# Optimization experiments

Measured on AMD Instinct MI355X. Metric: run time of the kernel, lower is better.

Reference implementation:

```python
import jax, jax.numpy as jnp
import numpy as np

L, H, DK = 4, 8, 64
NEG = -1e9
PAD = -9999.0


def _ln(z, g, b, eps=1e-6):
    # LayerNormalization: uses unbiased std (torch default) and divides by (std + eps)
    m = jnp.mean(z, axis=-1, keepdims=True)
    s = jnp.std(z, axis=-1, keepdims=True, ddof=1)
    return g * (z - m) / (s + eps) + b


def _mha(q_in, kv_in, w, bw, pw, pb, lnp, mask):
    B, Sq, D = q_in.shape
    q = (q_in @ w[0] + bw[0]).reshape(B, Sq, H, DK).transpose(0, 2, 1, 3)
    k = (kv_in @ w[1] + bw[1]).reshape(B, -1, H, DK).transpose(0, 2, 1, 3)
    v = (kv_in @ w[2] + bw[2]).reshape(B, -1, H, DK).transpose(0, 2, 1, 3)
    scores = jnp.einsum('bhqd,bhkd->bhqk', q, k) * (1.0 / np.sqrt(DK))
    if mask is not None:
        scores = jnp.where(mask[:, None, :, :], NEG, scores)
    attn = jax.nn.softmax(scores, axis=-1)
    ctx = jnp.einsum('bhqk,bhkd->bhqd', attn, v).transpose(0, 2, 1, 3).reshape(B, Sq, H * DK)
    return _ln(q_in + ctx @ pw + pb, lnp[0], lnp[1])


def _ffn(x, w1, b1, w2, b2, lnp):
    # kernel-1 conv1d == pointwise linear; w1:[d_ff,d_model], w2:[d_model,d_ff]
    h = jax.nn.relu(jnp.einsum('bsd,fd->bsf', x, w1) + b1)
    o = jnp.einsum('bsf,df->bsd', h, w2) + b2
    return _ln(x + o, lnp[0], lnp[1])


def _forward(enc_inputs, dec_inputs, emb_w, emb_b, pos_table,
             e_qkv_w, e_qkv_b, e_pw, e_pb, e_ln1, e_w1, e_b1, e_w2, e_b2, e_ln2,
             ds_qkv_w, ds_qkv_b, ds_pw, ds_pb, d_ln1,
             dc_qkv_w, dc_qkv_b, dc_pw, dc_pb, d_ln2,
             d_w1, d_b1, d_w2, d_b2, d_ln3):
    B, Se, F = enc_inputs.shape
    Sd = dec_inputs.shape[1]
    # ConvEmbeddingLayer: kernel-1 conv producing (d_model - n_features) channels, concat with raw inputs
    enc = jnp.concatenate([enc_inputs, jnp.einsum('bsf,of->bso', enc_inputs, emb_w) + emb_b], axis=-1)
    dec = jnp.concatenate([dec_inputs, jnp.einsum('bsf,of->bso', dec_inputs, emb_w) + emb_b], axis=-1)
    # PosEncoding with full lengths -> rows 1..S of the padded table
    enc = enc + pos_table[1:Se + 1]
    dec = dec + pos_table[1:Sd + 1]
    # masks per get_attn_pad_mask / get_attn_subsequent_mask
    enc_pad = jnp.sum(enc_inputs, axis=-1) <= PAD  # [B,Se]
    dec_pad = jnp.sum(dec_inputs, axis=-1) <= PAD  # [B,Sd]
    enc_mask = jnp.broadcast_to(enc_pad[:, None, :], (B, Se, Se))
    causal = jnp.triu(jnp.ones((Sd, Sd), dtype=bool), 1)
    dec_self_mask = jnp.broadcast_to(dec_pad[:, None, :], (B, Sd, Sd)) | causal
    cross_mask = jnp.broadcast_to(enc_pad[:, None, :], (B, Sd, Se))
    for i in range(L):
        enc = _mha(enc, enc, e_qkv_w[i], e_qkv_b[i], e_pw[i], e_pb[i], e_ln1[i], enc_mask)
        enc = _ffn(enc, e_w1[i], e_b1[i], e_w2[i], e_b2[i], e_ln2[i])
    for i in range(L):
        dec = _mha(dec, dec, ds_qkv_w[i], ds_qkv_b[i], ds_pw[i], ds_pb[i], d_ln1[i], dec_self_mask)
        dec = _mha(dec, enc, dc_qkv_w[i], dc_qkv_b[i], dc_pw[i], dc_pb[i], d_ln2[i], cross_mask)
        dec = _ffn(dec, d_w1[i], d_b1[i], d_w2[i], d_b2[i], d_ln3[i])
    return dec


def setup_inputs() -> dict:
    B, Se, Sd, F, Dm, Dff = 8, 512, 512, 32, 512, 2048
    key = jax.random.key(0)
    ks = iter(jax.random.split(key, 32))
    s = 0.02

    def n(shape, sc=s):
        return jax.random.normal(next(ks), shape, jnp.float32) * sc

    # sinusoidal PosEncoding table with leading pad row
    pos = np.arange(Se, dtype=np.float64)[:, None]
    j = np.arange(Dm)[None, :]
    ang = pos / np.power(10000.0, 2.0 * (j // 2) / Dm)
    ang[:, 0::2] = np.sin(ang[:, 0::2])
    ang[:, 1::2] = np.cos(ang[:, 1::2])
    pos_table = jnp.asarray(np.concatenate([np.zeros((1, Dm)), ang]).astype(np.float32))

    ln = jnp.broadcast_to(jnp.stack([jnp.ones(Dm), jnp.zeros(Dm)]), (L, 2, Dm)).astype(jnp.float32) + 0.0
    return {
        'enc_inputs': jax.random.normal(next(ks), (B, Se, F), jnp.float32),
        'dec_inputs': jax.random.normal(next(ks), (B, Sd, F), jnp.float32),
        'emb_w': n((Dm - F, F)), 'emb_b': jnp.zeros(Dm - F, jnp.float32),
        'pos_table': pos_table,
        'e_qkv_w': n((L, 3, Dm, H * DK)), 'e_qkv_b': jnp.zeros((L, 3, H * DK), jnp.float32),
        'e_pw': n((L, H * DK, Dm)), 'e_pb': jnp.zeros((L, Dm), jnp.float32), 'e_ln1': ln,
        'e_w1': n((L, Dff, Dm)), 'e_b1': jnp.zeros((L, Dff), jnp.float32),
        'e_w2': n((L, Dm, Dff)), 'e_b2': jnp.zeros((L, Dm), jnp.float32), 'e_ln2': ln,
        'ds_qkv_w': n((L, 3, Dm, H * DK)), 'ds_qkv_b': jnp.zeros((L, 3, H * DK), jnp.float32),
        'ds_pw': n((L, H * DK, Dm)), 'ds_pb': jnp.zeros((L, Dm), jnp.float32), 'd_ln1': ln,
        'dc_qkv_w': n((L, 3, Dm, H * DK)), 'dc_qkv_b': jnp.zeros((L, 3, H * DK), jnp.float32),
        'dc_pw': n((L, H * DK, Dm)), 'dc_pb': jnp.zeros((L, Dm), jnp.float32), 'd_ln2': ln,
        'd_w1': n((L, Dff, Dm)), 'd_b1': jnp.zeros((L, Dff), jnp.float32),
        'd_w2': n((L, Dm, Dff)), 'd_b2': jnp.zeros((L, Dm), jnp.float32), 'd_ln3': ln,
    }


def reference(enc_inputs, dec_inputs, emb_w, emb_b, pos_table,
              e_qkv_w, e_qkv_b, e_pw, e_pb, e_ln1, e_w1, e_b1, e_w2, e_b2, e_ln2,
              ds_qkv_w, ds_qkv_b, ds_pw, ds_pb, d_ln1,
              dc_qkv_w, dc_qkv_b, dc_pw, dc_pb, d_ln2,
              d_w1, d_b1, d_w2, d_b2, d_ln3):
    return _forward(enc_inputs, dec_inputs, emb_w, emb_b, pos_table,
                    e_qkv_w, e_qkv_b, e_pw, e_pb, e_ln1, e_w1, e_b1, e_w2, e_b2, e_ln2,
                    ds_qkv_w, ds_qkv_b, ds_pw, ds_pb, d_ln1,
                    dc_qkv_w, dc_qkv_b, dc_pw, dc_pb, d_ln2,
                    d_w1, d_b1, d_w2, d_b2, d_ln3)
```

## Files before the change

### kernel.cpp

```cpp
#include <hip/hip_runtime.h>
#include <cstdint>
#include <cstddef>

typedef unsigned short u16;
typedef __bf16 bf16x8 __attribute__((ext_vector_type(8)));
typedef float f32x4 __attribute__((ext_vector_type(4)));

constexpr int Bz = 8, Sq = 512, Hh = 8, DKd = 64, Dm = 512, Dff = 2048, NL = 4;
constexpr int TOK = Bz * Sq;
constexpr size_t MAT = (size_t)512 * 512;
constexpr size_t EL  = (size_t)TOK * Dm;
constexpr size_t WFT = (size_t)Dff * Dm;

__device__ __forceinline__ float bf2f(u16 u) {
  union { uint32_t i; float f; } v; v.i = (uint32_t)u << 16; return v.f;
}
__device__ __forceinline__ u16 f2bf(float f) {
  union { float f; uint32_t i; } v; v.f = f;
  uint32_t i = v.i;
  i += 0x7fffu + ((i >> 16) & 1u);
  return (u16)(i >> 16);
}

__device__ __forceinline__ void gload16(const u16* g, u16* l) {
  __builtin_amdgcn_global_load_lds(
      (const __attribute__((address_space(1))) unsigned int*)g,
      (__attribute__((address_space(3))) unsigned int*)l, 16, 0, 0);
}

template<int BM, int BN, int BK>
__global__ __launch_bounds__(256)
void gemm_tile(const u16* __restrict__ A, const u16* __restrict__ Bt,
               const float* __restrict__ bias, u16* __restrict__ C,
               int K, int lda, long long sA, int ldb, long long sB,
               int ldc, long long sC, int cmode, int relu, int colofs,
               const u16* A2, int xsplit)
{
  constexpr int HM = BM / 2, HN = BN / 2, MI = HM / 16, NI = HN / 16;
  constexpr int CPR = BK / 8;
  __shared__ __align__(16) u16 As[BM * BK];
  __shared__ __align__(16) u16 Bs[BN * BK];
  const int bz = blockIdx.z;
  const u16* Abase = A;
  int colbase;
  if (A2 && (int)blockIdx.x >= xsplit) {
    Abase = A2;
    colbase = 512 + ((int)blockIdx.x - xsplit) * BN;
  } else {
    colbase = colofs + (int)blockIdx.x * BN;
  }
  const u16* Ab = Abase + (size_t)bz * (size_t)sA + (size_t)(blockIdx.y * BM) * lda;
  const u16* Bb = Bt + (size_t)bz * (size_t)sB + (size_t)colbase * ldb;
  const int tid  = threadIdx.x;
  const int lane = tid & 63;
  const int wid  = tid >> 6;
  const int l15  = lane & 15;
  const int quad = lane >> 4;
  const int wm   = wid >> 1, wn = wid & 1;

  f32x4 acc[MI][NI] = {};

  for (int k0 = 0; k0 < K; k0 += BK) {
#pragma unroll
    for (int i = 0; i < (BM * CPR) / 256; ++i) {
      const int s = tid + i * 256;
      const int row = s / CPR, cl = s % CPR;
      const int c = (cl & 8) | ((cl ^ row) & 7);
      gload16(Ab + (size_t)row * lda + k0 + c * 8, As + s * 8);
    }
#pragma unroll
    for (int i = 0; i < (BN * CPR) / 256; ++i) {
      const int s = tid + i * 256;
      const int row = s / CPR, cl = s % CPR;
      const int c = (cl & 8) | ((cl ^ row) & 7);
      gload16(Bb + (size_t)row * ldb + k0 + c * 8, Bs + s * 8);
    }
    __syncthreads();
#pragma unroll
    for (int kk = 0; kk < BK / 32; ++kk) {
      bf16x8 af[MI], bfr[NI];
#pragma unroll
      for (int mi = 0; mi < MI; ++mi) {
        const int ra = wm * HM + mi * 16 + l15;
        const int ch = kk * 4 + quad;
        const int sw = (ch & 8) | ((ch ^ ra) & 7);
        af[mi] = *(const bf16x8*)(As + ra * BK + sw * 8);
      }
#pragma unroll
      for (int ni = 0; ni < NI; ++ni) {
        const int rb = wn * HN + ni * 16 + l15;
        const int ch = kk * 4 + quad;
        const int sw = (ch & 8) | ((ch ^ rb) & 7);
        bfr[ni] = *(const bf16x8*)(Bs + rb * BK + sw * 8);
      }
#pragma unroll
      for (int mi = 0; mi < MI; ++mi)
#pragma unroll
        for (int ni = 0; ni < NI; ++ni)
          acc[mi][ni] = __builtin_amdgcn_mfma_f32_16x16x32_bf16(af[mi], bfr[ni], acc[mi][ni], 0, 0, 0);
    }
    __syncthreads();
  }

  const int rblk = blockIdx.y * BM + wm * HM + quad * 4;
#pragma unroll
  for (int ni = 0; ni < NI; ++ni) {
    const int colx = colbase + wn * HN + ni * 16 + l15;
    const float bv = bias ? bias[colx] : 0.f;
#pragma unroll
    for (int mi = 0; mi < MI; ++mi) {
#pragma unroll
      for (int r = 0; r < 4; ++r) {
        float v = acc[mi][ni][r] + bv;
        if (relu) v = fmaxf(v, 0.f);
        const int grow = rblk + mi * 16 + r;
        size_t off;
        if (cmode == 0) {
          off = (size_t)bz * (size_t)sC + (size_t)grow * ldc + colx;
        } else {
          const int sec = colx >> 9, n = colx & 511, h = n >> 6, d = n & 63;
          const int b = grow >> 9, s = grow & 511;
          if (sec == 0) v *= 0.125f;
          if (sec < 2) off = (size_t)sec * EL + (size_t)b * 262144 + (size_t)h * 32768 + (size_t)s * 64 + d;
          else         off = 2 * EL + (size_t)b * 262144 + (size_t)h * 32768 + (size_t)d * 512 + s;
        }
        C[off] = f2bf(v);
      }
    }
  }
}

__global__ __launch_bounds__(256)
void flash_attn(const u16* __restrict__ q, const u16* __restrict__ k,
                const u16* __restrict__ v, const unsigned char* __restrict__ pad,
                u16* __restrict__ ctx, int mtype)
{
  __shared__ __align__(16) u16 KVs[8192];
  __shared__ __align__(16) u16 Pw[4][2048];
  const int bh = blockIdx.y, b = bh >> 3, h = bh & 7;
  const int qt = blockIdx.x;
  const int tid = threadIdx.x, lane = tid & 63, wid = tid >> 6;
  const int l15 = lane & 15, quad = lane >> 4;
  const size_t bho = (size_t)bh * 32768;
  const int qrow = qt * 64 + wid * 16 + l15;
  const int qcd  = qt * 64 + wid * 16 + quad * 4;

  unsigned char* Ps = (unsigned char*)&Pw[0][0];
  if (tid < 128) ((uchar4*)Ps)[tid] = ((const uchar4*)(pad + b * 512))[tid];

  bf16x8 aq0 = *(const bf16x8*)(q + bho + (size_t)qrow * 64 + quad * 8);
  bf16x8 aq1 = *(const bf16x8*)(q + bho + (size_t)qrow * 64 + 32 + quad * 8);

  f32x4 S[32];
#pragma unroll
  for (int kc = 0; kc < 4; ++kc) {
    __syncthreads();
#pragma unroll
    for (int i = 0; i < 4; ++i) {
      const int s = tid + i * 256;
      const int row = s >> 3, c = (s & 7) ^ (row & 7);
      gload16(k + bho + (size_t)(kc * 128 + row) * 64 + c * 8, KVs + s * 8);
    }
    __syncthreads();
#pragma unroll
    for (int t = 0; t < 8; ++t) {
      const int sw = l15 & 7;
      bf16x8 b0 = *(const bf16x8*)(KVs + (t * 16 + l15) * 64 + (quad ^ sw) * 8);
      bf16x8 b1 = *(const bf16x8*)(KVs + (t * 16 + l15) * 64 + ((4 + quad) ^ sw) * 8);
      f32x4 z = {0.f, 0.f, 0.f, 0.f};
      z = __builtin_amdgcn_mfma_f32_16x16x32_bf16(aq0, b0, z, 0, 0, 0);
      S[kc * 8 + t] = __builtin_amdgcn_mfma_f32_16x16x32_bf16(aq1, b1, z, 0, 0, 0);
    }
  }

  unsigned pm = 0u;
#pragma unroll
  for (int t = 0; t < 32; ++t) pm |= (unsigned)(Ps[t * 16 + l15] != 0) << t;

  float inv[4];
#pragma unroll
  for (int r = 0; r < 4; ++r) {
    const int qg = qcd + r;
    float mx = -3.0e38f;
#pragma unroll
    for (int t = 0; t < 32; ++t) {
      const int col = t * 16 + l15;
      const bool m = ((pm >> t) & 1u) || (mtype == 1 && col > qg);
      const float val = m ? -1e9f : S[t][r];
      S[t][r] = val;
      mx = fmaxf(mx, val);
    }
#pragma unroll
    for (int o = 8; o > 0; o >>= 1) mx = fmaxf(mx, __shfl_xor(mx, o));
    float sm = 0.f;
#pragma unroll
    for (int t = 0; t < 32; ++t) { const float e = __expf(S[t][r] - mx); S[t][r] = e; sm += e; }
#pragma unroll
    for (int o = 8; o > 0; o >>= 1) sm += __shfl_xor(sm, o);
    inv[r] = 1.f / sm;
  }

  f32x4 O[4] = {};
  u16* myP = &Pw[wid][0];
#pragma unroll
  for (int kc = 0; kc < 4; ++kc) {
    __syncthreads();
#pragma unroll
    for (int i = 0; i < 4; ++i) {
      const int s = tid + i * 256;
      const int row = s >> 4, c = (s & 15) ^ (row & 15);
      gload16(v + bho + (size_t)row * 512 + kc * 128 + c * 8, KVs + s * 8);
    }
#pragma unroll
    for (int t = 0; t < 8; ++t)
#pragma unroll
      for (int r = 0; r < 4; ++r) {
        const int rowq = quad * 4 + r;
        const int c = 2 * t + (l15 >> 3);
        myP[rowq * 128 + (c ^ rowq) * 8 + (l15 & 7)] = f2bf(S[kc * 8 + t][r] * inv[r]);
      }
    __syncthreads();
#pragma unroll
    for (int kk = 0; kk < 4; ++kk) {
      bf16x8 ap = *(const bf16x8*)(myP + l15 * 128 + ((kk * 4 + quad) ^ l15) * 8);
#pragma unroll
      for (int ni = 0; ni < 4; ++ni) {
        bf16x8 bv = *(const bf16x8*)(KVs + (ni * 16 + l15) * 128 + ((kk * 4 + quad) ^ l15) * 8);
        O[ni] = __builtin_amdgcn_mfma_f32_16x16x32_bf16(ap, bv, O[ni], 0, 0, 0);
      }
    }
  }

  const int token = b * 512 + qcd;
#pragma unroll
  for (int ni = 0; ni < 4; ++ni)
#pragma unroll
    for (int r = 0; r < 4; ++r)
      ctx[(size_t)(token + r) * 512 + h * 64 + ni * 16 + l15] = f2bf(O[ni][r]);
}

__global__ __launch_bounds__(256)
void prep_weights(const float* __restrict__ s0, const float* __restrict__ s1,
                  const float* __restrict__ s2, const float* __restrict__ s3,
                  const float* __restrict__ s4, const float* __restrict__ s5,
                  u16* __restrict__ outT,
                  const float* __restrict__ c0, const float* __restrict__ c1,
                  const float* __restrict__ c2, const float* __restrict__ c3,
                  u16* __restrict__ outC)
{
  __shared__ float tile[32][33];
  const int z = blockIdx.z;
  if (z < 48) {
    const float* src; int zi;
    if      (z < 12) { src = s0; zi = z; }
    else if (z < 24) { src = s1; zi = z - 12; }
    else if (z < 36) { src = s2; zi = z - 24; }
    else if (z < 40) { src = s3; zi = z - 36; }
    else if (z < 44) { src = s4; zi = z - 40; }
    else             { src = s5; zi = z - 44; }
    const float* in = src + (size_t)zi * MAT;
    u16* o = outT + (size_t)z * MAT;
    int x = blockIdx.x * 32 + threadIdx.x;
    int y = blockIdx.y * 32 + threadIdx.y;
#pragma unroll
    for (int i = 0; i < 32; i += 8)
      tile[threadIdx.y + i][threadIdx.x] = in[(size_t)(y + i) * 512 + x];
    __syncthreads();
    x = blockIdx.y * 32 + threadIdx.x;
    y = blockIdx.x * 32 + threadIdx.y;
#pragma unroll
    for (int i = 0; i < 32; i += 8)
      o[(size_t)(y + i) * 512 + x] = f2bf(tile[threadIdx.x][threadIdx.y + i]);
  } else {
    const int tid = threadIdx.y * 32 + threadIdx.x;
    const int L = (z - 48) * 256 + blockIdx.y * 16 + blockIdx.x;
    const int tens = L >> 12, bx = L & 4095;
    const float* srcs[4] = { c0, c1, c2, c3 };
    const float* src = srcs[tens];
    u16* dst = outC + (size_t)tens * (4 * WFT);
    const int i = (bx * 256 + tid) * 4;
    float4 v = *(const float4*)(src + i);
    ushort4 u = { f2bf(v.x), f2bf(v.y), f2bf(v.z), f2bf(v.w) };
    *(ushort4*)(dst + i) = u;
  }
}

__global__ __launch_bounds__(256)
void embed2(const float* __restrict__ xe, const float* __restrict__ xd,
            const float* __restrict__ ew, const float* __restrict__ eb,
            const float* __restrict__ pos,
            u16* __restrict__ oute, u16* __restrict__ outd,
            unsigned char* __restrict__ pe, unsigned char* __restrict__ pd)
{
  const float* x = blockIdx.y ? xd : xe;
  u16* out = blockIdx.y ? outd : oute;
  unsigned char* padv = blockIdx.y ? pd : pe;
  const int rs = blockIdx.x;
  const int s  = rs & 511;
  __shared__ float xr[32];
  const int t = threadIdx.x;
  if (t < 32) xr[t] = x[(size_t)rs * 32 + t];
  __syncthreads();
  if (t == 0) {
    float sacc = 0.f;
#pragma unroll
    for (int f = 0; f < 32; ++f) sacc += xr[f];
    padv[rs] = (sacc <= -9999.f) ? 1 : 0;
  }
#pragma unroll
  for (int rep = 0; rep < 2; ++rep) {
    const int c = t + rep * 256;
    float v;
    if (c < 32) {
      v = xr[c];
    } else {
      const float* w = ew + (size_t)(c - 32) * 32;
      float acc = eb[c - 32];
#pragma unroll
      for (int f = 0; f < 32; ++f) acc += xr[f] * w[f];
      v = acc;
    }
    v += pos[(size_t)(s + 1) * 512 + c];
    out[(size_t)rs * 512 + c] = f2bf(v);
  }
}

__global__ __launch_bounds__(256)
void add_ln(const u16* __restrict__ x, const u16* __restrict__ y,
            const float* __restrict__ g, const float* __restrict__ bb,
            u16* __restrict__ out, float* __restrict__ out32)
{
  const int row  = blockIdx.x * 4 + (threadIdx.x >> 6);
  const int lane = threadIdx.x & 63;
  const int c0 = lane * 8;
  const size_t base = (size_t)row * Dm + c0;

  uint4 xr = *(const uint4*)(x + base);
  uint4 yr = *(const uint4*)(y + base);
  const u16* xh = (const u16*)&xr;
  const u16* yh = (const u16*)&yr;
  float z[8];
  float s = 0.f;
#pragma unroll
  for (int j = 0; j < 8; ++j) { z[j] = bf2f(xh[j]) + bf2f(yh[j]); s += z[j]; }
#pragma unroll
  for (int off = 32; off > 0; off >>= 1) s += __shfl_xor(s, off);
  const float mean = s * (1.f / 512.f);
  float ss = 0.f;
#pragma unroll
  for (int j = 0; j < 8; ++j) { z[j] -= mean; ss += z[j] * z[j]; }
#pragma unroll
  for (int off = 32; off > 0; off >>= 1) ss += __shfl_xor(ss, off);
  const float stdv = sqrtf(ss * (1.f / 511.f));
  const float inv = 1.f / (stdv + 1e-6f);

  float4 g0 = *(const float4*)(g + c0),  g1 = *(const float4*)(g + c0 + 4);
  float4 b0 = *(const float4*)(bb + c0), b1 = *(const float4*)(bb + c0 + 4);
  float gv[8] = { g0.x, g0.y, g0.z, g0.w, g1.x, g1.y, g1.z, g1.w };
  float bv[8] = { b0.x, b0.y, b0.z, b0.w, b1.x, b1.y, b1.z, b1.w };
  float o[8];
#pragma unroll
  for (int j = 0; j < 8; ++j) o[j] = gv[j] * z[j] * inv + bv[j];
  if (out32) {
    float4 w0 = { o[0], o[1], o[2], o[3] };
    float4 w1 = { o[4], o[5], o[6], o[7] };
    *(float4*)(out32 + base) = w0;
    *(float4*)(out32 + base + 4) = w1;
  } else {
    uint4 ow;
    u16* oh = (u16*)&ow;
#pragma unroll
    for (int j = 0; j < 8; ++j) oh[j] = f2bf(o[j]);
    *(uint4*)(out + base) = ow;
  }
}

extern "C" void kernel_launch(void* const* d_in, const int* in_sizes, int n_in,
                              void* d_out, int out_size, void* d_ws, size_t ws_size,
                              hipStream_t stream)
{
  (void)in_sizes; (void)n_in; (void)out_size;
  const float* enc_in   = (const float*)d_in[0];
  const float* dec_in   = (const float*)d_in[1];
  const float* emb_w    = (const float*)d_in[2];
  const float* emb_b    = (const float*)d_in[3];
  const float* pos      = (const float*)d_in[4];
  const float* e_qkv_w  = (const float*)d_in[5];
  const float* e_qkv_b  = (const float*)d_in[6];
  const float* e_pw     = (const float*)d_in[7];
  const float* e_pb     = (const float*)d_in[8];
  const float* e_ln1    = (const float*)d_in[9];
  const float* e_w1     = (const float*)d_in[10];
  const float* e_b1     = (const float*)d_in[11];
  const float* e_w2     = (const float*)d_in[12];
  const float* e_b2     = (const float*)d_in[13];
  const float* e_ln2    = (const float*)d_in[14];
  const float* ds_qkv_w = (const float*)d_in[15];
  const float* ds_qkv_b = (const float*)d_in[16];
  const float* ds_pw    = (const float*)d_in[17];
  const float* ds_pb    = (const float*)d_in[18];
  const float* d_ln1    = (const float*)d_in[19];
  const float* dc_qkv_w = (const float*)d_in[20];
  const float* dc_qkv_b = (const float*)d_in[21];
  const float* dc_pw    = (const float*)d_in[22];
  const float* dc_pb    = (const float*)d_in[23];
  const float* d_ln2    = (const float*)d_in[24];
  const float* d_w1     = (const float*)d_in[25];
  const float* d_b1     = (const float*)d_in[26];
  const float* d_w2     = (const float*)d_in[27];
  const float* d_b2     = (const float*)d_in[28];
  const float* d_ln3    = (const float*)d_in[29];

  u16* ws  = (u16*)d_ws;
  u16* enc = ws;
  u16* dec = ws + EL;
  u16* qb  = ws + 2 * EL;
  u16* kb  = ws + 3 * EL;
  u16* vT  = ws + 4 * EL;
  u16* ctx = ws + 5 * EL;
  u16* t1  = ws + 6 * EL;
  u16* hff = ws + 7 * EL;
  u16* wT  = ws + 15 * EL;
  unsigned char* padE = (unsigned char*)(ws + 21 * EL);
  unsigned char* padD = padE + TOK;
  u16* wfAll = ws + 22 * EL;
  if (ws_size < 30 * EL * 2 + 2 * TOK) return;

  prep_weights<<<dim3(16, 16, 112), dim3(32, 8), 0, stream>>>(
      e_qkv_w, ds_qkv_w, dc_qkv_w, e_pw, ds_pw, dc_pw, wT,
      e_w1, e_w2, d_w1, d_w2, wfAll);
  embed2<<<dim3(TOK, 2), 256, 0, stream>>>(enc_in, dec_in, emb_w, emb_b, pos,
                                           enc, dec, padE, padD);

  auto attention = [&](const u16* qsrc, const u16* kvsrc, const u16* wq3, const float* b3,
                       const u16* pwT, const float* pb, const float* ln,
                       const unsigned char* pad, int mtype, u16* x) {
    if (qsrc == kvsrc) {
      gemm_tile<64, 128, 128><<<dim3(12, 64, 1), 256, 0, stream>>>(
          qsrc, wq3, b3, qb, 512, 512, 0, 512, 0, 0, 0, 4, 0, 0, nullptr, 0);
    } else {
      gemm_tile<64, 128, 128><<<dim3(12, 64, 1), 256, 0, stream>>>(
          qsrc, wq3, b3, qb, 512, 512, 0, 512, 0, 0, 0, 4, 0, 0, kvsrc, 4);
    }
    flash_attn<<<dim3(8, 64), 256, 0, stream>>>(qb, kb, vT, pad, ctx, mtype);
    gemm_tile<64, 64, 128><<<dim3(8, 64, 1), 256, 0, stream>>>(
        ctx, pwT, pb, t1, 512, 512, 0, 512, 0, 512, 0, 0, 0, 0, nullptr, 0);
    add_ln<<<TOK / 4, 256, 0, stream>>>(x, t1, ln, ln + 512, x, nullptr);
  };

  auto ffn = [&](u16* x, const u16* w1b, const float* b1, const u16* w2b,
                 const float* b2, const float* ln, float* o32) {
    gemm_tile<64, 128, 128><<<dim3(16, 64, 1), 256, 0, stream>>>(
        x, w1b, b1, hff, 512, 512, 0, 512, 0, 2048, 0, 0, 1, 0, nullptr, 0);
    gemm_tile<64, 64, 128><<<dim3(8, 64, 1), 256, 0, stream>>>(
        hff, w2b, b2, t1, 2048, 2048, 0, 2048, 0, 512, 0, 0, 0, 0, nullptr, 0);
    add_ln<<<TOK / 4, 256, 0, stream>>>(x, t1, ln, ln + 512, x, o32);
  };

  for (int i = 0; i < NL; ++i) {
    attention(enc, enc, wT + (size_t)(i * 3) * MAT, e_qkv_b + i * 3 * 512,
              wT + (size_t)(36 + i) * MAT, e_pb + i * 512, e_ln1 + i * 1024, padE, 0, enc);
    ffn(enc, wfAll + (size_t)i * WFT, e_b1 + i * Dff,
        wfAll + 4 * WFT + (size_t)i * WFT, e_b2 + i * Dm, e_ln2 + i * 1024, nullptr);
  }

  for (int i = 0; i < NL; ++i) {
    attention(dec, dec, wT + (size_t)(12 + i * 3) * MAT, ds_qkv_b + i * 3 * 512,
              wT + (size_t)(40 + i) * MAT, ds_pb + i * 512, d_ln1 + i * 1024, padD, 1, dec);
    attention(dec, enc, wT + (size_t)(24 + i * 3) * MAT, dc_qkv_b + i * 3 * 512,
              wT + (size_t)(44 + i) * MAT, dc_pb + i * 512, d_ln2 + i * 1024, padE, 2, dec);
    ffn(dec, wfAll + 8 * WFT + (size_t)i * WFT, d_b1 + i * Dff,
        wfAll + 12 * WFT + (size_t)i * WFT, d_b2 + i * Dm, d_ln3 + i * 1024,
        (i == NL - 1) ? (float*)d_out : nullptr);
  }
}
```

Baseline: 1.311 ms.

## Shrink GEMM K-tile to 64, enlarge FFN1 tile, and turn embedding into a GEMM

```diff
diff --git a/kernel.cpp b/kernel.cpp
--- a/kernel.cpp
+++ b/kernel.cpp
@@ -28,18 +28,17 @@
       (__attribute__((address_space(3))) unsigned int*)l, 16, 0, 0);
 }
 
-template<int BM, int BN, int BK>
+template<int BM, int BN>
 __global__ __launch_bounds__(256)
 void gemm_tile(const u16* __restrict__ A, const u16* __restrict__ Bt,
                const float* __restrict__ bias, u16* __restrict__ C,
                int K, int lda, long long sA, int ldb, long long sB,
                int ldc, long long sC, int cmode, int relu, int colofs,
-               const u16* A2, int xsplit)
+               const u16* A2, int xsplit, const float* __restrict__ posp)
 {
   constexpr int HM = BM / 2, HN = BN / 2, MI = HM / 16, NI = HN / 16;
-  constexpr int CPR = BK / 8;
-  __shared__ __align__(16) u16 As[BM * BK];
-  __shared__ __align__(16) u16 Bs[BN * BK];
+  __shared__ __align__(16) u16 As[BM * 64];
+  __shared__ __align__(16) u16 Bs[BN * 64];
   const int bz = blockIdx.z;
   const u16* Abase = A;
   int colbase;
@@ -60,38 +59,32 @@
 
   f32x4 acc[MI][NI] = {};
 
-  for (int k0 = 0; k0 < K; k0 += BK) {
-#pragma unroll
-    for (int i = 0; i < (BM * CPR) / 256; ++i) {
+  for (int k0 = 0; k0 < K; k0 += 64) {
+#pragma unroll
+    for (int i = 0; i < BM / 32; ++i) {
       const int s = tid + i * 256;
-      const int row = s / CPR, cl = s % CPR;
-      const int c = (cl & 8) | ((cl ^ row) & 7);
+      const int row = s >> 3, c = (s & 7) ^ (row & 7);
       gload16(Ab + (size_t)row * lda + k0 + c * 8, As + s * 8);
     }
 #pragma unroll
-    for (int i = 0; i < (BN * CPR) / 256; ++i) {
+    for (int i = 0; i < BN / 32; ++i) {
       const int s = tid + i * 256;
-      const int row = s / CPR, cl = s % CPR;
-      const int c = (cl & 8) | ((cl ^ row) & 7);
+      const int row = s >> 3, c = (s & 7) ^ (row & 7);
       gload16(Bb + (size_t)row * ldb + k0 + c * 8, Bs + s * 8);
     }
     __syncthreads();
 #pragma unroll
-    for (int kk = 0; kk < BK / 32; ++kk) {
+    for (int kk = 0; kk < 2; ++kk) {
       bf16x8 af[MI], bfr[NI];
 #pragma unroll
       for (int mi = 0; mi < MI; ++mi) {
         const int ra = wm * HM + mi * 16 + l15;
-        const int ch = kk * 4 + quad;
-        const int sw = (ch & 8) | ((ch ^ ra) & 7);
-        af[mi] = *(const bf16x8*)(As + ra * BK + sw * 8);
+        af[mi] = *(const bf16x8*)(As + ra * 64 + (((kk * 4 + quad) ^ (ra & 7))) * 8);
       }
 #pragma unroll
       for (int ni = 0; ni < NI; ++ni) {
         const int rb = wn * HN + ni * 16 + l15;
-        const int ch = kk * 4 + quad;
-        const int sw = (ch & 8) | ((ch ^ rb) & 7);
-        bfr[ni] = *(const bf16x8*)(Bs + rb * BK + sw * 8);
+        bfr[ni] = *(const bf16x8*)(Bs + rb * 64 + (((kk * 4 + quad) ^ (rb & 7))) * 8);
       }
 #pragma unroll
       for (int mi = 0; mi < MI; ++mi)
@@ -117,6 +110,10 @@
         size_t off;
         if (cmode == 0) {
           off = (size_t)bz * (size_t)sC + (size_t)grow * ldc + colx;
+        } else if (cmode == 5) {
+          const int s = grow & 511;
+          v += posp[(size_t)(s + 1) * 512 + colx];
+          off = (size_t)grow * 512 + colx;
         } else {
           const int sec = colx >> 9, n = colx & 511, h = n >> 6, d = n & 63;
           const int b = grow >> 9, s = grow & 511;
@@ -246,7 +243,9 @@
                   u16* __restrict__ outT,
                   const float* __restrict__ c0, const float* __restrict__ c1,
                   const float* __restrict__ c2, const float* __restrict__ c3,
-                  u16* __restrict__ outC)
+                  u16* __restrict__ outC,
+                  const float* __restrict__ ew, const float* __restrict__ eb,
+                  u16* __restrict__ ewb, float* __restrict__ biasE)
 {
   __shared__ float tile[32][33];
   const int z = blockIdx.z;
@@ -271,7 +270,7 @@
 #pragma unroll
     for (int i = 0; i < 32; i += 8)
       o[(size_t)(y + i) * 512 + x] = f2bf(tile[threadIdx.x][threadIdx.y + i]);
-  } else {
+  } else if (z < 112) {
     const int tid = threadIdx.y * 32 + threadIdx.x;
     const int L = (z - 48) * 256 + blockIdx.y * 16 + blockIdx.x;
     const int tens = L >> 12, bx = L & 4095;
@@ -282,47 +281,47 @@
     float4 v = *(const float4*)(src + i);
     ushort4 u = { f2bf(v.x), f2bf(v.y), f2bf(v.z), f2bf(v.w) };
     *(ushort4*)(dst + i) = u;
+  } else {
+    const int tid = threadIdx.y * 32 + threadIdx.x;
+    const int bxy = blockIdx.y * 16 + blockIdx.x;
+    if (tid < 128) {
+      const int row = bxy * 2 + (tid >> 6);
+      const int c = tid & 63;
+      float v;
+      if (row < 32) v = (c == row) ? 1.f : 0.f;
+      else          v = (c < 32) ? ew[(size_t)(row - 32) * 32 + c] : 0.f;
+      ewb[(size_t)row * 64 + c] = f2bf(v);
+    }
+    if (bxy == 0) {
+#pragma unroll
+      for (int rep = 0; rep < 2; ++rep) {
+        const int i = tid + rep * 256;
+        biasE[i] = (i < 32) ? 0.f : eb[i - 32];
+      }
+    }
   }
 }
 
 __global__ __launch_bounds__(256)
-void embed2(const float* __restrict__ xe, const float* __restrict__ xd,
-            const float* __restrict__ ew, const float* __restrict__ eb,
-            const float* __restrict__ pos,
-            u16* __restrict__ oute, u16* __restrict__ outd,
-            unsigned char* __restrict__ pe, unsigned char* __restrict__ pd)
-{
-  const float* x = blockIdx.y ? xd : xe;
-  u16* out = blockIdx.y ? outd : oute;
-  unsigned char* padv = blockIdx.y ? pd : pe;
-  const int rs = blockIdx.x;
-  const int s  = rs & 511;
-  __shared__ float xr[32];
-  const int t = threadIdx.x;
-  if (t < 32) xr[t] = x[(size_t)rs * 32 + t];
-  __syncthreads();
-  if (t == 0) {
-    float sacc = 0.f;
-#pragma unroll
-    for (int f = 0; f < 32; ++f) sacc += xr[f];
-    padv[rs] = (sacc <= -9999.f) ? 1 : 0;
-  }
-#pragma unroll
-  for (int rep = 0; rep < 2; ++rep) {
-    const int c = t + rep * 256;
-    float v;
-    if (c < 32) {
-      v = xr[c];
-    } else {
-      const float* w = ew + (size_t)(c - 32) * 32;
-      float acc = eb[c - 32];
-#pragma unroll
-      for (int f = 0; f < 32; ++f) acc += xr[f] * w[f];
-      v = acc;
-    }
-    v += pos[(size_t)(s + 1) * 512 + c];
-    out[(size_t)rs * 512 + c] = f2bf(v);
-  }
+void embed_pre(const float* __restrict__ xe, const float* __restrict__ xd,
+               u16* __restrict__ xbf,
+               unsigned char* __restrict__ pe, unsigned char* __restrict__ pd)
+{
+  const int r = blockIdx.x * 8 + (threadIdx.x >> 5);
+  const int lw = threadIdx.x & 31;
+  const float* x = (r < 4096) ? xe : xd;
+  const int rr = r & 4095;
+  const float v = x[(size_t)rr * 32 + lw];
+  float sm = v;
+#pragma unroll
+  for (int o = 16; o > 0; o >>= 1) sm += __shfl_xor(sm, o);
+  if (lw == 0) {
+    unsigned char* pv = (r < 4096) ? pe : pd;
+    pv[rr] = (sm <= -9999.f) ? 1 : 0;
+  }
+  u16* o = xbf + (size_t)r * 64;
+  o[lw] = f2bf(v);
+  o[32 + lw] = 0;
 }
 
 __global__ __launch_bounds__(256)
@@ -423,37 +422,42 @@
   u16* wT  = ws + 15 * EL;
   unsigned char* padE = (unsigned char*)(ws + 21 * EL);
   unsigned char* padD = padE + TOK;
+  u16* xbf   = ws + 21 * EL + 8192;
+  u16* ewb   = xbf + (size_t)8192 * 64;
+  float* biasE = (float*)(ewb + 32768);
   u16* wfAll = ws + 22 * EL;
   if (ws_size < 30 * EL * 2 + 2 * TOK) return;
 
-  prep_weights<<<dim3(16, 16, 112), dim3(32, 8), 0, stream>>>(
+  prep_weights<<<dim3(16, 16, 113), dim3(32, 8), 0, stream>>>(
       e_qkv_w, ds_qkv_w, dc_qkv_w, e_pw, ds_pw, dc_pw, wT,
-      e_w1, e_w2, d_w1, d_w2, wfAll);
-  embed2<<<dim3(TOK, 2), 256, 0, stream>>>(enc_in, dec_in, emb_w, emb_b, pos,
-                                           enc, dec, padE, padD);
+      e_w1, e_w2, d_w1, d_w2, wfAll,
+      emb_w, emb_b, ewb, biasE);
+  embed_pre<<<1024, 256, 0, stream>>>(enc_in, dec_in, xbf, padE, padD);
+  gemm_tile<64, 128><<<dim3(4, 128, 1), 256, 0, stream>>>(
+      xbf, ewb, biasE, enc, 64, 64, 0, 64, 0, 512, 0, 5, 0, 0, nullptr, 0, pos);
 
   auto attention = [&](const u16* qsrc, const u16* kvsrc, const u16* wq3, const float* b3,
                        const u16* pwT, const float* pb, const float* ln,
                        const unsigned char* pad, int mtype, u16* x) {
     if (qsrc == kvsrc) {
-      gemm_tile<64, 128, 128><<<dim3(12, 64, 1), 256, 0, stream>>>(
-          qsrc, wq3, b3, qb, 512, 512, 0, 512, 0, 0, 0, 4, 0, 0, nullptr, 0);
+      gemm_tile<64, 128><<<dim3(12, 64, 1), 256, 0, stream>>>(
+          qsrc, wq3, b3, qb, 512, 512, 0, 512, 0, 0, 0, 4, 0, 0, nullptr, 0, nullptr);
     } else {
-      gemm_tile<64, 128, 128><<<dim3(12, 64, 1), 256, 0, stream>>>(
-          qsrc, wq3, b3, qb, 512, 512, 0, 512, 0, 0, 0, 4, 0, 0, kvsrc, 4);
+      gemm_tile<64, 128><<<dim3(12, 64, 1), 256, 0, stream>>>(
+          qsrc, wq3, b3, qb, 512, 512, 0, 512, 0, 0, 0, 4, 0, 0, kvsrc, 4, nullptr);
     }
     flash_attn<<<dim3(8, 64), 256, 0, stream>>>(qb, kb, vT, pad, ctx, mtype);
-    gemm_tile<64, 64, 128><<<dim3(8, 64, 1), 256, 0, stream>>>(
-        ctx, pwT, pb, t1, 512, 512, 0, 512, 0, 512, 0, 0, 0, 0, nullptr, 0);
+    gemm_tile<64, 64><<<dim3(8, 64, 1), 256, 0, stream>>>(
+        ctx, pwT, pb, t1, 512, 512, 0, 512, 0, 512, 0, 0, 0, 0, nullptr, 0, nullptr);
     add_ln<<<TOK / 4, 256, 0, stream>>>(x, t1, ln, ln + 512, x, nullptr);
   };
 
   auto ffn = [&](u16* x, const u16* w1b, const float* b1, const u16* w2b,
                  const float* b2, const float* ln, float* o32) {
-    gemm_tile<64, 128, 128><<<dim3(16, 64, 1), 256, 0, stream>>>(
-        x, w1b, b1, hff, 512, 512, 0, 512, 0, 2048, 0, 0, 1, 0, nullptr, 0);
-    gemm_tile<64, 64, 128><<<dim3(8, 64, 1), 256, 0, stream>>>(
-        hff, w2b, b2, t1, 2048, 2048, 0, 2048, 0, 512, 0, 0, 0, 0, nullptr, 0);
+    gemm_tile<128, 128><<<dim3(16, 32, 1), 256, 0, stream>>>(
+        x, w1b, b1, hff, 512, 512, 0, 512, 0, 2048, 0, 0, 1, 0, nullptr, 0, nullptr);
+    gemm_tile<64, 64><<<dim3(8, 64, 1), 256, 0, stream>>>(
+        hff, w2b, b2, t1, 2048, 2048, 0, 2048, 0, 512, 0, 0, 0, 0, nullptr, 0, nullptr);
     add_ln<<<TOK / 4, 256, 0, stream>>>(x, t1, ln, ln + 512, x, o32);
   };
 
```

Result: no change. 1.290 ms (-1.6%).
